# Kernel optimization log

Hardware: AMD Instinct MI355X
Metric: run time of the kernel (lower is better)

## Reference

```python
import jax, jax.numpy as jnp
import numpy as np

SPARSITY = 0.5  # cur_sparsity set during training; 0.0 default would make masking a no-op
WEIGHT_BETA = 1.0
MASK_ALPHA1 = 1.0
MASK_ALPHA2 = 1.0


def binarize(mask_scores, sparsity):
    # SparseBinarizer.forward: prune (set to 0) the `num_prune` smallest scores globally.
    num_prune = int(mask_scores.size * sparsity)  # static: sparsity is a Python float
    flat = mask_scores.reshape(-1)
    prune_idx = jnp.argsort(flat)[:num_prune]
    mask = jnp.ones_like(flat).at[prune_idx].set(0.0)
    return mask.reshape(mask_scores.shape)


def setup_inputs() -> dict:
    key = jax.random.key(0)
    ks = jax.random.split(key, 9)
    out_f, in_f, r = 4096, 4096, 8
    tokens = 8192  # batch 4 * seq 2048
    return {
        "x": jax.random.normal(ks[0], (tokens, in_f), dtype=jnp.float32),
        "weight": jax.random.normal(ks[1], (out_f, in_f), dtype=jnp.float32) * 0.02,
        "bias": jax.random.normal(ks[2], (out_f,), dtype=jnp.float32) * 0.02,
        "weight_U": jax.random.normal(ks[3], (out_f, r), dtype=jnp.float32),
        "weight_V": jnp.zeros((r, in_f), dtype=jnp.float32),
        "mask_scores_A": jax.random.normal(ks[4], (out_f, r), dtype=jnp.float32),
        "mask_scores_B": jnp.zeros((r, in_f), dtype=jnp.float32),
        "mask_scores_R": jnp.zeros((out_f,), dtype=jnp.float32),
        "mask_scores_C": jnp.zeros((in_f,), dtype=jnp.float32),
    }


def reference(x, weight, bias, weight_U, weight_V, mask_scores_A, mask_scores_B,
              mask_scores_R, mask_scores_C):
    # weight = W + beta * U @ V   (low-rank weight reconstruction)
    w = weight + WEIGHT_BETA * (weight_U @ weight_V)
    # mask_scores = |w| + a1 * A @ B + a2 * (R[:,None] + C[None,:])
    mask_scores = (jnp.abs(w)
                   + MASK_ALPHA1 * (mask_scores_A @ mask_scores_B)
                   + MASK_ALPHA2 * (mask_scores_R[:, None] + mask_scores_C[None, :]))
    mask = binarize(mask_scores, SPARSITY)
    masked_weight = mask * w  # [out_f, in_f]
    # nn.Linear: x @ W^T + b
    return x @ masked_weight.T + bias
```

## Files before the change

### kernel.cpp

```cpp
#include <hip/hip_runtime.h>
#include <stdint.h>

#define TOKENS 8192
#define OUT_F  4096
#define IN_F   4096
#define RNK    8
#define KPRUNE 8388608u
#define CAP3   16384u

typedef unsigned short u16;
typedef float  f32x4  __attribute__((ext_vector_type(4)));
typedef short  bf16x8 __attribute__((ext_vector_type(8)));
typedef unsigned short u16x4 __attribute__((ext_vector_type(4)));
typedef unsigned short u16x8 __attribute__((ext_vector_type(8)));

#define XB_OFF    0ull
#define WB_OFF    67108864ull
#define KEYS_OFF  100663296ull
#define CTL_OFF   167772160ull
#define H1_OFF    0
#define H2_OFF    16384
#define SEL_OFF   32768
#define CNT3_OFF  32800
#define LIST3_OFF 32804
#define CTL_ZERO_U32 8201

__device__ __forceinline__ u16 f2bf(float f) {
    uint32_t u = __float_as_uint(f);
    u += 0x7fffu + ((u >> 16) & 1u);
    return (u16)(u >> 16);
}

__device__ __forceinline__ uint32_t fkey(float s) {
    uint32_t u = __float_as_uint(s);
    return (u & 0x80000000u) ? ~u : (u | 0x80000000u);
}

__global__ void convx_kernel(const float* __restrict__ x, u16* __restrict__ xB,
                             uint32_t* __restrict__ ctl)
{
    const int t = threadIdx.x;
    if (blockIdx.x < 34) {
        const int i = blockIdx.x * 256 + t;
        if (i < CTL_ZERO_U32) ctl[i] = 0u;
    }
    const size_t idx = (size_t)blockIdx.x * 256 + t;
    const float4* xv = (const float4*)x;
    float4 a = xv[idx*2];
    float4 b = xv[idx*2 + 1];
    u16x8 o;
    o[0]=f2bf(a.x); o[1]=f2bf(a.y); o[2]=f2bf(a.z); o[3]=f2bf(a.w);
    o[4]=f2bf(b.x); o[5]=f2bf(b.y); o[6]=f2bf(b.z); o[7]=f2bf(b.w);
    *((u16x8*)xB + idx) = o;
}

__global__ void prep_kernel(const float* __restrict__ W, const float* __restrict__ U,
                            const float* __restrict__ V, const float* __restrict__ A,
                            const float* __restrict__ B, const float* __restrict__ R,
                            const float* __restrict__ C, u16* __restrict__ wB,
                            uint32_t* __restrict__ keys, uint32_t* __restrict__ hist1)
{
    __shared__ uint32_t lh[4096];
    const int o0 = blockIdx.x * 2, t = threadIdx.x;
    for (int b = t; b < 4096; b += 256) lh[b] = 0u;
    float uu0[RNK], uu1[RNK], aa0[RNK], aa1[RNK];
#pragma unroll
    for (int r = 0; r < RNK; ++r) {
        uu0[r] = U[o0*RNK + r];       uu1[r] = U[(o0+1)*RNK + r];
        aa0[r] = A[o0*RNK + r];       aa1[r] = A[(o0+1)*RNK + r];
    }
    const float ro0 = R[o0], ro1 = R[o0 + 1];
    __syncthreads();
    for (int j = 0; j < IN_F/1024; ++j) {
        const int i = j*1024 + t*4;
        const float4 cc = *(const float4*)&C[i];
        float4 w0 = *(const float4*)&W[(size_t)o0*IN_F + i];
        float4 w1 = *(const float4*)&W[(size_t)(o0+1)*IN_F + i];
#pragma unroll
        for (int r = 0; r < RNK; ++r) {
            const float4 v4 = *(const float4*)&V[r*IN_F + i];
            const float a0 = uu0[r], a1 = uu1[r];
            w0.x = fmaf(a0, v4.x, w0.x); w0.y = fmaf(a0, v4.y, w0.y);
            w0.z = fmaf(a0, v4.z, w0.z); w0.w = fmaf(a0, v4.w, w0.w);
            w1.x = fmaf(a1, v4.x, w1.x); w1.y = fmaf(a1, v4.y, w1.y);
            w1.z = fmaf(a1, v4.z, w1.z); w1.w = fmaf(a1, v4.w, w1.w);
        }
        float4 s0, s1;
        s0.x = fabsf(w0.x); s0.y = fabsf(w0.y); s0.z = fabsf(w0.z); s0.w = fabsf(w0.w);
        s1.x = fabsf(w1.x); s1.y = fabsf(w1.y); s1.z = fabsf(w1.z); s1.w = fabsf(w1.w);
#pragma unroll
        for (int r = 0; r < RNK; ++r) {
            const float4 b4 = *(const float4*)&B[r*IN_F + i];
            const float a0 = aa0[r], a1 = aa1[r];
            s0.x = fmaf(a0, b4.x, s0.x); s0.y = fmaf(a0, b4.y, s0.y);
            s0.z = fmaf(a0, b4.z, s0.z); s0.w = fmaf(a0, b4.w, s0.w);
            s1.x = fmaf(a1, b4.x, s1.x); s1.y = fmaf(a1, b4.y, s1.y);
            s1.z = fmaf(a1, b4.z, s1.z); s1.w = fmaf(a1, b4.w, s1.w);
        }
        s0.x += ro0 + cc.x; s0.y += ro0 + cc.y; s0.z += ro0 + cc.z; s0.w += ro0 + cc.w;
        s1.x += ro1 + cc.x; s1.y += ro1 + cc.y; s1.z += ro1 + cc.z; s1.w += ro1 + cc.w;
        uint4 k0, k1;
        k0.x = fkey(s0.x); k0.y = fkey(s0.y); k0.z = fkey(s0.z); k0.w = fkey(s0.w);
        k1.x = fkey(s1.x); k1.y = fkey(s1.y); k1.z = fkey(s1.z); k1.w = fkey(s1.w);
        *(uint4*)&keys[(size_t)o0*IN_F + i]     = k0;
        *(uint4*)&keys[(size_t)(o0+1)*IN_F + i] = k1;
        u16x4 b0, b1;
        b0[0]=f2bf(w0.x); b0[1]=f2bf(w0.y); b0[2]=f2bf(w0.z); b0[3]=f2bf(w0.w);
        b1[0]=f2bf(w1.x); b1[1]=f2bf(w1.y); b1[2]=f2bf(w1.z); b1[3]=f2bf(w1.w);
        *(u16x4*)&wB[(size_t)o0*IN_F + i]     = b0;
        *(u16x4*)&wB[(size_t)(o0+1)*IN_F + i] = b1;
        atomicAdd(&lh[k0.x >> 20], 1u); atomicAdd(&lh[k0.y >> 20], 1u);
        atomicAdd(&lh[k0.z >> 20], 1u); atomicAdd(&lh[k0.w >> 20], 1u);
        atomicAdd(&lh[k1.x >> 20], 1u); atomicAdd(&lh[k1.y >> 20], 1u);
        atomicAdd(&lh[k1.z >> 20], 1u); atomicAdd(&lh[k1.w >> 20], 1u);
    }
    __syncthreads();
    for (int b = t; b < 4096; b += 256) { uint32_t c = lh[b]; if (c) atomicAdd(&hist1[b], c); }
}

__global__ void select_kernel(const uint32_t* __restrict__ hist, uint32_t* sel, int mode)
{
    __shared__ uint32_t lh[4096];
    __shared__ uint32_t part[256];
    __shared__ uint32_t sseg[2];
    const int t = threadIdx.x;
    const uint32_t c1v = sel[1];
    const uint32_t k = (mode == 0) ? KPRUNE : (KPRUNE - c1v);
    for (int b = t; b < 4096; b += 256) lh[b] = hist[b];
    __syncthreads();
    uint32_t s = 0;
    for (int j = 0; j < 16; ++j) s += lh[t*16 + j];
    part[t] = s;
    __syncthreads();
    uint32_t pre = 0;
    for (int tt = 0; tt < t; ++tt) pre += part[tt];
    if (pre < k && pre + part[t] >= k) { sseg[0] = (uint32_t)t; sseg[1] = pre; }
    __syncthreads();
    const int seg = (int)sseg[0];
    const uint32_t accb = sseg[1];
    if (t < 16) {
        uint32_t pre2 = 0;
        for (int j = 0; j < t; ++j) pre2 += lh[seg*16 + j];
        const uint32_t c = lh[seg*16 + t];
        const uint32_t below = accb + pre2;
        if (below < k && below + c >= k) {
            const uint32_t bin = (uint32_t)(seg*16 + t);
            if (mode == 0) { sel[0] = bin; sel[1] = below; }
            else           { sel[2] = bin; sel[3] = c1v + below; }
        }
    }
}

__global__ void hist2_kernel(const uint32_t* __restrict__ keys, const uint32_t* __restrict__ sel,
                             uint32_t* __restrict__ hist2)
{
    __shared__ uint32_t lh[4096];
    const int o = blockIdx.x, t = threadIdx.x;
    const uint32_t b1 = sel[0];
    for (int b = t; b < 4096; b += 256) lh[b] = 0u;
    __syncthreads();
    const uint32_t* kp = keys + (size_t)o*IN_F + t*16;
#pragma unroll
    for (int q = 0; q < 4; ++q) {
        uint4 kv = *(const uint4*)(kp + q*4);
        if ((kv.x >> 20) == b1) atomicAdd(&lh[(kv.x >> 8) & 0xFFFu], 1u);
        if ((kv.y >> 20) == b1) atomicAdd(&lh[(kv.y >> 8) & 0xFFFu], 1u);
        if ((kv.z >> 20) == b1) atomicAdd(&lh[(kv.z >> 8) & 0xFFFu], 1u);
        if ((kv.w >> 20) == b1) atomicAdd(&lh[(kv.w >> 8) & 0xFFFu], 1u);
    }
    __syncthreads();
    for (int b = t; b < 4096; b += 256) { uint32_t c = lh[b]; if (c) atomicAdd(&hist2[b], c); }
}

__global__ void apply_kernel(const uint32_t* __restrict__ keys, const uint32_t* __restrict__ sel,
                             u16* __restrict__ wB, uint32_t* __restrict__ cnt3,
                             uint32_t* __restrict__ list3)
{
    const uint32_t pfx = (sel[0] << 12) | sel[2];
    const size_t base = ((size_t)blockIdx.x * 256 + threadIdx.x) * 16;
    uint32_t kv[16];
#pragma unroll
    for (int q = 0; q < 4; ++q) *(uint4*)(kv + q*4) = *(const uint4*)(keys + base + q*4);
    uint4 wraw[2];
    wraw[0] = *(const uint4*)(wB + base);
    wraw[1] = *(const uint4*)(wB + base + 8);
    u16* wv = (u16*)wraw;
#pragma unroll
    for (int e = 0; e < 16; ++e) {
        const uint32_t hi = kv[e] >> 8;
        if (hi < pfx) wv[e] = 0u;
        else if (hi == pfx) {
            uint32_t s = atomicAdd(cnt3, 1u);
            if (s < CAP3) list3[s] = ((uint32_t)(base + e) << 8) | (kv[e] & 0xFFu);
        }
    }
    *(uint4*)(wB + base)     = wraw[0];
    *(uint4*)(wB + base + 8) = wraw[1];
}

__global__ void selfix_kernel(const uint32_t* __restrict__ sel, const uint32_t* __restrict__ cnt3,
                              const uint32_t* __restrict__ list3, u16* __restrict__ wB)
{
    __shared__ uint32_t lst[CAP3];
    __shared__ uint32_t hist[256];
    __shared__ uint32_t sv[2];
    const int t = threadIdx.x;
    uint32_t n = *cnt3; if (n > CAP3) n = CAP3;
    hist[t] = 0u;
    __syncthreads();
    for (uint32_t i = t; i < n; i += 256) {
        const uint32_t e = list3[i];
        lst[i] = e;
        atomicAdd(&hist[e & 0xFFu], 1u);
    }
    __syncthreads();
    const uint32_t k3 = KPRUNE - sel[3];
    uint32_t pre = 0;
    for (int b = 0; b < t; ++b) pre += hist[b];
    if (pre < k3 && pre + hist[t] >= k3) {
        sv[0] = (uint32_t)t;
        sv[1] = k3 - pre;
    }
    __syncthreads();
    const uint32_t b3 = sv[0], p = sv[1];
    for (uint32_t i = t; i < n; i += 256) {
        const uint32_t e = lst[i];
        const uint32_t lo = e & 0xFFu;
        if (lo < b3) { wB[e >> 8] = 0u; continue; }
        if (lo != b3) continue;
        uint32_t rank = 0;
        for (uint32_t j = 0; j < n; ++j) {
            const uint32_t f = lst[j];
            rank += ((f & 0xFFu) == b3 && f < e) ? 1u : 0u;
        }
        if (rank < p) wB[e >> 8] = 0u;
    }
}

#define A0H0   0
#define A0H1_0 16384
#define A0H1_1 32768
#define B0S    49152
#define A1H0   81920
#define A1H1_0 98304
#define A1H1_1 114688
#define B1S    131072

__device__ __forceinline__ void gl_lds16(const char* src, char* dst) {
    __builtin_amdgcn_global_load_lds((const __attribute__((address_space(1))) void*)src,
                                     (__attribute__((address_space(3))) void*)dst, 16, 0, 0);
}

__global__ __launch_bounds__(512, 2) void gemm256_kernel(const u16* __restrict__ xB,
                                                         const u16* __restrict__ wB,
                                                         const float* __restrict__ bias,
                                                         float* __restrict__ out)
{
    __shared__ char ldsc[163840];
    const int t    = threadIdx.x;
    const int lane = t & 63;
    const int wid  = t >> 6;
    const int wm   = wid >> 2;
    const int wn   = wid & 3;
    const int bid  = blockIdx.x;
    const int bn   = bid & 15;
    const int bm   = bid >> 4;

    const int l15 = lane & 15;
    const int kb  = (lane >> 4) << 4;
    const int rowA = 16*wm + l15;
    const int rowB = (wn & 1)*64 + l15;
    const int baseA = rowA*64 + (kb ^ (((rowA >> 1) & 3) << 4));
    const int baseB = rowB*64 + (kb ^ (((rowB >> 1) & 3) << 4));
    const char* aB0 = ldsc + baseA;
    const char* aB1 = ldsc + A1H0 + baseA;
    const char* bB0 = ldsc + B0S + (wn >> 1)*16384 + baseB;
    const char* bB1 = bB0 + (B1S - B0S);

    const int scol = ((t & 3) * 16) ^ (((t >> 3) & 3) << 4);
    const char* pA = (const char*)xB + ((size_t)(bm*256 + (t >> 2))) * (IN_F*2) + scol;
    const char* pB = (const char*)wB + ((size_t)(bn*256 + (t >> 2))) * (IN_F*2) + scol;
    const int tb16 = t * 16;

#define STAGEH(pG, slot, h, tile) do {                                        \
    const char* _s = (pG) + (size_t)(tile)*128 + (size_t)(h)*(128*IN_F*2);    \
    char* _d = ldsc + (slot) + tb16;                                          \
    gl_lds16(_s, _d);                                                         \
    gl_lds16(_s + 64, _d + 8192);                                             \
} while (0)

    f32x4  acc[8][4] = {};
    bf16x8 b[4][2];
    bf16x8 a[2][2];

#define LOADB(bp) do {                                                        \
    _Pragma("unroll") for (int ni = 0; ni < 4; ++ni)                          \
    _Pragma("unroll") for (int kk = 0; kk < 2; ++kk)                          \
        b[ni][kk] = *(const bf16x8*)((bp) + ni*1024 + kk*8192);               \
} while (0)

#define LOADA(ap, slot, q, mo) do {                                           \
    _Pragma("unroll") for (int mm = 0; mm < 2; ++mm)                          \
    _Pragma("unroll") for (int kk = 0; kk < 2; ++kk)                          \
        a[mm][kk] = *(const bf16x8*)((ap) + (slot) +                          \
                      (2*(q)+mm-(mo))*2048 + kk*8192);                        \
} while (0)

#define MFMAQ(q) do {                                                         \
    _Pragma("unroll") for (int mm = 0; mm < 2; ++mm)                          \
    _Pragma("unroll") for (int ni = 0; ni < 4; ++ni)                          \
    _Pragma("unroll") for (int kk = 0; kk < 2; ++kk)                          \
        acc[2*(q)+mm][ni] = __builtin_amdgcn_mfma_f32_16x16x32_bf16(          \
            a[mm][kk], b[ni][kk], acc[2*(q)+mm][ni], 0, 0, 0);                \
} while (0)

#define PH_TAIL(q)                                                            \
    __builtin_amdgcn_s_barrier();                                             \
    asm volatile("s_waitcnt lgkmcnt(0)" ::: "memory");                        \
    __builtin_amdgcn_s_setprio(1);                                            \
    MFMAQ(q);                                                                 \
    __builtin_amdgcn_s_setprio(0);                                            \
    __builtin_amdgcn_s_barrier();

#define STQ(q) do {                                                           \
    _Pragma("unroll") for (int mm = 0; mm < 2; ++mm) {                        \
        const int r0 = orow0 + 32*(2*(q)+mm);                                 \
        _Pragma("unroll") for (int ni = 0; ni < 4; ++ni) {                    \
            f32x4 v = acc[2*(q)+mm][ni];                                      \
            const int col = ocol0 + ni*16;                                    \
            _Pragma("unroll") for (int e = 0; e < 4; ++e)                     \
                out[(size_t)(r0 + e)*OUT_F + col] = v[e] + bv[ni];            \
        }                                                                     \
    }                                                                         \
} while (0)

#define PH_TAIL_ST(q)                                                         \
    __builtin_amdgcn_s_barrier();                                             \
    asm volatile("s_waitcnt lgkmcnt(0)" ::: "memory");                        \
    __builtin_amdgcn_s_setprio(1);                                            \
    MFMAQ(q);                                                                 \
    __builtin_amdgcn_s_setprio(0);                                            \
    STQ(q);                                                                   \
    __builtin_amdgcn_s_barrier();

    STAGEH(pA, A0H1_0, 1, 0);
    STAGEH(pB, B0S,         0, 0);
    STAGEH(pB, B0S + 16384, 1, 0);
    STAGEH(pA, A0H0, 0, 0);
    STAGEH(pA, A1H1_0, 1, 1);
    STAGEH(pB, B1S,         0, 1);
    STAGEH(pB, B1S + 16384, 1, 1);
    STAGEH(pA, A1H0, 0, 1);
    asm volatile("s_waitcnt vmcnt(8)" ::: "memory");
    __builtin_amdgcn_s_barrier();

#pragma unroll 1
    for (int j = 0; j < 31; ++j) {
        const int se = 2*j + 2;
        const int so = 2*j + 3;
        const int pc = j & 1;
        const int a0h1c = pc ? A0H1_1 : A0H1_0;
        const int a0h1n = pc ? A0H1_0 : A0H1_1;
        const int a1h1c = pc ? A1H1_1 : A1H1_0;
        const int a1h1n = pc ? A1H1_0 : A1H1_1;

        LOADB(bB0); LOADA(aB0, A0H0, 0, 0);
        STAGEH(pA, a0h1n, 1, se);
        asm volatile("s_waitcnt lgkmcnt(8)" ::: "memory");
        PH_TAIL(0)
        LOADA(aB0, A0H0, 1, 0);
        STAGEH(pB, B0S, 0, se);
        PH_TAIL(1)
        LOADA(aB0, a0h1c, 2, 4);
        STAGEH(pB, B0S + 16384, 1, se);
        PH_TAIL(2)
        LOADA(aB0, a0h1c, 3, 4);
        STAGEH(pA, A0H0, 0, se);
        asm volatile("s_waitcnt vmcnt(8)" ::: "memory");
        PH_TAIL(3)

        LOADB(bB1); LOADA(aB1, 0, 0, 0);
        STAGEH(pA, a1h1n, 1, so);
        asm volatile("s_waitcnt lgkmcnt(8)" ::: "memory");
        PH_TAIL(0)
        LOADA(aB1, 0, 1, 0);
        STAGEH(pB, B1S, 0, so);
        PH_TAIL(1)
        LOADA(aB1, a1h1c - A1H0, 2, 4);
        STAGEH(pB, B1S + 16384, 1, so);
        PH_TAIL(2)
        LOADA(aB1, a1h1c - A1H0, 3, 4);
        STAGEH(pA, A1H0, 0, so);
        asm volatile("s_waitcnt vmcnt(8)" ::: "memory");
        PH_TAIL(3)
    }

    const int orow0 = bm*256 + 16*wm + ((lane >> 4) << 2);
    const int ocol0 = bn*256 + 64*wn + l15;
    float bv[4];
#pragma unroll
    for (int ni = 0; ni < 4; ++ni) bv[ni] = bias[ocol0 + ni*16];

    LOADB(bB0); LOADA(aB0, A0H0, 0, 0);
    asm volatile("s_waitcnt lgkmcnt(8)" ::: "memory");
    PH_TAIL(0)
    LOADA(aB0, A0H0, 1, 0);
    PH_TAIL(1)
    LOADA(aB0, A0H1_1, 2, 4);
    PH_TAIL(2)
    LOADA(aB0, A0H1_1, 3, 4);
    PH_TAIL(3)

    asm volatile("s_waitcnt vmcnt(0)" ::: "memory");
    __builtin_amdgcn_s_barrier();
    LOADB(bB1); LOADA(aB1, 0, 0, 0);
    asm volatile("s_waitcnt lgkmcnt(8)" ::: "memory");
    PH_TAIL_ST(0)
    LOADA(aB1, 0, 1, 0);
    PH_TAIL_ST(1)
    LOADA(aB1, A1H1_1 - A1H0, 2, 4);
    PH_TAIL_ST(2)
    LOADA(aB1, A1H1_1 - A1H0, 3, 4);
    PH_TAIL_ST(3)

#undef STAGEH
#undef LOADB
#undef LOADA
#undef MFMAQ
#undef PH_TAIL
#undef PH_TAIL_ST
#undef STQ
}

extern "C" void kernel_launch(void* const* d_in, const int* in_sizes, int n_in,
                              void* d_out, int out_size, void* d_ws, size_t ws_size,
                              hipStream_t stream)
{
    const float* x    = (const float*)d_in[0];
    const float* W    = (const float*)d_in[1];
    const float* bias = (const float*)d_in[2];
    const float* U    = (const float*)d_in[3];
    const float* V    = (const float*)d_in[4];
    const float* A    = (const float*)d_in[5];
    const float* B    = (const float*)d_in[6];
    const float* R    = (const float*)d_in[7];
    const float* C    = (const float*)d_in[8];
    float* out = (float*)d_out;

    char* ws = (char*)d_ws;
    u16*      xB    = (u16*)(ws + XB_OFF);
    u16*      wB    = (u16*)(ws + WB_OFF);
    uint32_t* keys  = (uint32_t*)(ws + KEYS_OFF);
    uint32_t* ctl   = (uint32_t*)(ws + CTL_OFF);
    uint32_t* h1    = (uint32_t*)((char*)ctl + H1_OFF);
    uint32_t* h2    = (uint32_t*)((char*)ctl + H2_OFF);
    uint32_t* sel   = (uint32_t*)((char*)ctl + SEL_OFF);
    uint32_t* cnt3  = (uint32_t*)((char*)ctl + CNT3_OFF);
    uint32_t* list3 = (uint32_t*)((char*)ctl + LIST3_OFF);

    convx_kernel<<<TOKENS*IN_F/8/256, 256, 0, stream>>>(x, xB, ctl);
    prep_kernel<<<OUT_F/2, 256, 0, stream>>>(W, U, V, A, B, R, C, wB, keys, h1);
    select_kernel<<<1, 256, 0, stream>>>(h1, sel, 0);
    hist2_kernel<<<OUT_F, 256, 0, stream>>>(keys, sel, h2);
    select_kernel<<<1, 256, 0, stream>>>(h2, sel, 1);
    apply_kernel<<<OUT_F, 256, 0, stream>>>(keys, sel, wB, cnt3, list3);
    selfix_kernel<<<1, 256, 0, stream>>>(sel, cnt3, list3, wB);
    gemm256_kernel<<<(TOKENS/256)*(OUT_F/256), 512, 0, stream>>>(xB, wB, bias, out);
}
```

Measured before the change: 400.4 us.

## Recompute mask scores from inputs instead of storing and rereading key buffer

The 64MB intermediate keys array is removed. Each selection pass (histogram, second histogram, apply) recomputes the low-rank weight and mask scores directly from W, U, V, A, B, R, C. The bf16 weight is now written only once, in the apply pass, which drops the separate write plus read-modify-write of wB. This replaces one 64MB key write and two 64MB key reads with two extra 64MB reads of W and some redundant FMA work.

```diff
diff --git a/kernel.cpp b/kernel.cpp
--- a/kernel.cpp
+++ b/kernel.cpp
@@ -16,8 +16,7 @@
 
 #define XB_OFF    0ull
 #define WB_OFF    67108864ull
-#define KEYS_OFF  100663296ull
-#define CTL_OFF   167772160ull
+#define CTL_OFF   100663296ull
 #define H1_OFF    0
 #define H2_OFF    16384
 #define SEL_OFF   32768
@@ -35,6 +34,56 @@
     uint32_t u = __float_as_uint(s);
     return (u & 0x80000000u) ? ~u : (u | 0x80000000u);
 }
+
+struct S2 { float4 w0, w1; uint4 k0, k1; };
+__device__ __forceinline__ S2 score2(const float* __restrict__ W,
+                                     const float* __restrict__ V,
+                                     const float* __restrict__ B,
+                                     const float* __restrict__ C,
+                                     const float* uu0, const float* uu1,
+                                     const float* aa0, const float* aa1,
+                                     float ro0, float ro1, int o0, int i)
+{
+    const float4 cc = *(const float4*)&C[i];
+    float4 w0 = *(const float4*)&W[(size_t)o0*IN_F + i];
+    float4 w1 = *(const float4*)&W[(size_t)(o0+1)*IN_F + i];
+#pragma unroll
+    for (int r = 0; r < RNK; ++r) {
+        const float4 v4 = *(const float4*)&V[r*IN_F + i];
+        const float a0 = uu0[r], a1 = uu1[r];
+        w0.x = fmaf(a0, v4.x, w0.x); w0.y = fmaf(a0, v4.y, w0.y);
+        w0.z = fmaf(a0, v4.z, w0.z); w0.w = fmaf(a0, v4.w, w0.w);
+        w1.x = fmaf(a1, v4.x, w1.x); w1.y = fmaf(a1, v4.y, w1.y);
+        w1.z = fmaf(a1, v4.z, w1.z); w1.w = fmaf(a1, v4.w, w1.w);
+    }
+    float4 s0, s1;
+    s0.x = fabsf(w0.x); s0.y = fabsf(w0.y); s0.z = fabsf(w0.z); s0.w = fabsf(w0.w);
+    s1.x = fabsf(w1.x); s1.y = fabsf(w1.y); s1.z = fabsf(w1.z); s1.w = fabsf(w1.w);
+#pragma unroll
+    for (int r = 0; r < RNK; ++r) {
+        const float4 b4 = *(const float4*)&B[r*IN_F + i];
+        const float a0 = aa0[r], a1 = aa1[r];
+        s0.x = fmaf(a0, b4.x, s0.x); s0.y = fmaf(a0, b4.y, s0.y);
+        s0.z = fmaf(a0, b4.z, s0.z); s0.w = fmaf(a0, b4.w, s0.w);
+        s1.x = fmaf(a1, b4.x, s1.x); s1.y = fmaf(a1, b4.y, s1.y);
+        s1.z = fmaf(a1, b4.z, s1.z); s1.w = fmaf(a1, b4.w, s1.w);
+    }
+    s0.x += ro0 + cc.x; s0.y += ro0 + cc.y; s0.z += ro0 + cc.z; s0.w += ro0 + cc.w;
+    s1.x += ro1 + cc.x; s1.y += ro1 + cc.y; s1.z += ro1 + cc.z; s1.w += ro1 + cc.w;
+    S2 o;
+    o.w0 = w0; o.w1 = w1;
+    o.k0.x = fkey(s0.x); o.k0.y = fkey(s0.y); o.k0.z = fkey(s0.z); o.k0.w = fkey(s0.w);
+    o.k1.x = fkey(s1.x); o.k1.y = fkey(s1.y); o.k1.z = fkey(s1.z); o.k1.w = fkey(s1.w);
+    return o;
+}
+
+#define LOAD_ROWPARAMS                                                        \
+    float uu0[RNK], uu1[RNK], aa0[RNK], aa1[RNK];                             \
+    _Pragma("unroll") for (int r = 0; r < RNK; ++r) {                         \
+        uu0[r] = U[o0*RNK + r];   uu1[r] = U[(o0+1)*RNK + r];                 \
+        aa0[r] = A[o0*RNK + r];   aa1[r] = A[(o0+1)*RNK + r];                 \
+    }                                                                         \
+    const float ro0 = R[o0], ro1 = R[o0 + 1];
 
 __global__ void convx_kernel(const float* __restrict__ x, u16* __restrict__ xB,
                              uint32_t* __restrict__ ctl)
@@ -57,62 +106,20 @@
 __global__ void prep_kernel(const float* __restrict__ W, const float* __restrict__ U,
                             const float* __restrict__ V, const float* __restrict__ A,
                             const float* __restrict__ B, const float* __restrict__ R,
-                            const float* __restrict__ C, u16* __restrict__ wB,
-                            uint32_t* __restrict__ keys, uint32_t* __restrict__ hist1)
+                            const float* __restrict__ C, uint32_t* __restrict__ hist1)
 {
     __shared__ uint32_t lh[4096];
     const int o0 = blockIdx.x * 2, t = threadIdx.x;
     for (int b = t; b < 4096; b += 256) lh[b] = 0u;
-    float uu0[RNK], uu1[RNK], aa0[RNK], aa1[RNK];
-#pragma unroll
-    for (int r = 0; r < RNK; ++r) {
-        uu0[r] = U[o0*RNK + r];       uu1[r] = U[(o0+1)*RNK + r];
-        aa0[r] = A[o0*RNK + r];       aa1[r] = A[(o0+1)*RNK + r];
-    }
-    const float ro0 = R[o0], ro1 = R[o0 + 1];
+    LOAD_ROWPARAMS
     __syncthreads();
     for (int j = 0; j < IN_F/1024; ++j) {
         const int i = j*1024 + t*4;
-        const float4 cc = *(const float4*)&C[i];
-        float4 w0 = *(const float4*)&W[(size_t)o0*IN_F + i];
-        float4 w1 = *(const float4*)&W[(size_t)(o0+1)*IN_F + i];
-#pragma unroll
-        for (int r = 0; r < RNK; ++r) {
-            const float4 v4 = *(const float4*)&V[r*IN_F + i];
-            const float a0 = uu0[r], a1 = uu1[r];
-            w0.x = fmaf(a0, v4.x, w0.x); w0.y = fmaf(a0, v4.y, w0.y);
-            w0.z = fmaf(a0, v4.z, w0.z); w0.w = fmaf(a0, v4.w, w0.w);
-            w1.x = fmaf(a1, v4.x, w1.x); w1.y = fmaf(a1, v4.y, w1.y);
-            w1.z = fmaf(a1, v4.z, w1.z); w1.w = fmaf(a1, v4.w, w1.w);
-        }
-        float4 s0, s1;
-        s0.x = fabsf(w0.x); s0.y = fabsf(w0.y); s0.z = fabsf(w0.z); s0.w = fabsf(w0.w);
-        s1.x = fabsf(w1.x); s1.y = fabsf(w1.y); s1.z = fabsf(w1.z); s1.w = fabsf(w1.w);
-#pragma unroll
-        for (int r = 0; r < RNK; ++r) {
-            const float4 b4 = *(const float4*)&B[r*IN_F + i];
-            const float a0 = aa0[r], a1 = aa1[r];
-            s0.x = fmaf(a0, b4.x, s0.x); s0.y = fmaf(a0, b4.y, s0.y);
-            s0.z = fmaf(a0, b4.z, s0.z); s0.w = fmaf(a0, b4.w, s0.w);
-            s1.x = fmaf(a1, b4.x, s1.x); s1.y = fmaf(a1, b4.y, s1.y);
-            s1.z = fmaf(a1, b4.z, s1.z); s1.w = fmaf(a1, b4.w, s1.w);
-        }
-        s0.x += ro0 + cc.x; s0.y += ro0 + cc.y; s0.z += ro0 + cc.z; s0.w += ro0 + cc.w;
-        s1.x += ro1 + cc.x; s1.y += ro1 + cc.y; s1.z += ro1 + cc.z; s1.w += ro1 + cc.w;
-        uint4 k0, k1;
-        k0.x = fkey(s0.x); k0.y = fkey(s0.y); k0.z = fkey(s0.z); k0.w = fkey(s0.w);
-        k1.x = fkey(s1.x); k1.y = fkey(s1.y); k1.z = fkey(s1.z); k1.w = fkey(s1.w);
-        *(uint4*)&keys[(size_t)o0*IN_F + i]     = k0;
-        *(uint4*)&keys[(size_t)(o0+1)*IN_F + i] = k1;
-        u16x4 b0, b1;
-        b0[0]=f2bf(w0.x); b0[1]=f2bf(w0.y); b0[2]=f2bf(w0.z); b0[3]=f2bf(w0.w);
-        b1[0]=f2bf(w1.x); b1[1]=f2bf(w1.y); b1[2]=f2bf(w1.z); b1[3]=f2bf(w1.w);
-        *(u16x4*)&wB[(size_t)o0*IN_F + i]     = b0;
-        *(u16x4*)&wB[(size_t)(o0+1)*IN_F + i] = b1;
-        atomicAdd(&lh[k0.x >> 20], 1u); atomicAdd(&lh[k0.y >> 20], 1u);
-        atomicAdd(&lh[k0.z >> 20], 1u); atomicAdd(&lh[k0.w >> 20], 1u);
-        atomicAdd(&lh[k1.x >> 20], 1u); atomicAdd(&lh[k1.y >> 20], 1u);
-        atomicAdd(&lh[k1.z >> 20], 1u); atomicAdd(&lh[k1.w >> 20], 1u);
+        S2 s = score2(W, V, B, C, uu0, uu1, aa0, aa1, ro0, ro1, o0, i);
+        atomicAdd(&lh[s.k0.x >> 20], 1u); atomicAdd(&lh[s.k0.y >> 20], 1u);
+        atomicAdd(&lh[s.k0.z >> 20], 1u); atomicAdd(&lh[s.k0.w >> 20], 1u);
+        atomicAdd(&lh[s.k1.x >> 20], 1u); atomicAdd(&lh[s.k1.y >> 20], 1u);
+        atomicAdd(&lh[s.k1.z >> 20], 1u); atomicAdd(&lh[s.k1.w >> 20], 1u);
     }
     __syncthreads();
     for (int b = t; b < 4096; b += 256) { uint32_t c = lh[b]; if (c) atomicAdd(&hist1[b], c); }
@@ -151,51 +158,73 @@
     }
 }
 
-__global__ void hist2_kernel(const uint32_t* __restrict__ keys, const uint32_t* __restrict__ sel,
-                             uint32_t* __restrict__ hist2)
+__global__ void hist2r_kernel(const float* __restrict__ W, const float* __restrict__ U,
+                              const float* __restrict__ V, const float* __restrict__ A,
+                              const float* __restrict__ B, const float* __restrict__ R,
+                              const float* __restrict__ C, const uint32_t* __restrict__ sel,
+                              uint32_t* __restrict__ hist2)
 {
     __shared__ uint32_t lh[4096];
-    const int o = blockIdx.x, t = threadIdx.x;
+    const int o0 = blockIdx.x * 2, t = threadIdx.x;
     const uint32_t b1 = sel[0];
     for (int b = t; b < 4096; b += 256) lh[b] = 0u;
-    __syncthreads();
-    const uint32_t* kp = keys + (size_t)o*IN_F + t*16;
+    LOAD_ROWPARAMS
+    __syncthreads();
+    for (int j = 0; j < IN_F/1024; ++j) {
+        const int i = j*1024 + t*4;
+        S2 s = score2(W, V, B, C, uu0, uu1, aa0, aa1, ro0, ro1, o0, i);
+        if ((s.k0.x >> 20) == b1) atomicAdd(&lh[(s.k0.x >> 8) & 0xFFFu], 1u);
+        if ((s.k0.y >> 20) == b1) atomicAdd(&lh[(s.k0.y >> 8) & 0xFFFu], 1u);
+        if ((s.k0.z >> 20) == b1) atomicAdd(&lh[(s.k0.z >> 8) & 0xFFFu], 1u);
+        if ((s.k0.w >> 20) == b1) atomicAdd(&lh[(s.k0.w >> 8) & 0xFFFu], 1u);
+        if ((s.k1.x >> 20) == b1) atomicAdd(&lh[(s.k1.x >> 8) & 0xFFFu], 1u);
+        if ((s.k1.y >> 20) == b1) atomicAdd(&lh[(s.k1.y >> 8) & 0xFFFu], 1u);
+        if ((s.k1.z >> 20) == b1) atomicAdd(&lh[(s.k1.z >> 8) & 0xFFFu], 1u);
+        if ((s.k1.w >> 20) == b1) atomicAdd(&lh[(s.k1.w >> 8) & 0xFFFu], 1u);
+    }
+    __syncthreads();
+    for (int b = t; b < 4096; b += 256) { uint32_t c = lh[b]; if (c) atomicAdd(&hist2[b], c); }
+}
+
+__global__ void applyr_kernel(const float* __restrict__ W, const float* __restrict__ U,
+                              const float* __restrict__ V, const float* __restrict__ A,
+                              const float* __restrict__ B, const float* __restrict__ R,
+                              const float* __restrict__ C, const uint32_t* __restrict__ sel,
+                              u16* __restrict__ wB, uint32_t* __restrict__ cnt3,
+                              uint32_t* __restrict__ list3)
+{
+    const int o0 = blockIdx.x * 2, t = threadIdx.x;
+    const uint32_t pfx = (sel[0] << 12) | sel[2];
+    LOAD_ROWPARAMS
+    for (int j = 0; j < IN_F/1024; ++j) {
+        const int i = j*1024 + t*4;
+        S2 s = score2(W, V, B, C, uu0, uu1, aa0, aa1, ro0, ro1, o0, i);
+        const float w0a[4] = {s.w0.x, s.w0.y, s.w0.z, s.w0.w};
+        const float w1a[4] = {s.w1.x, s.w1.y, s.w1.z, s.w1.w};
+        const uint32_t k0a[4] = {s.k0.x, s.k0.y, s.k0.z, s.k0.w};
+        const uint32_t k1a[4] = {s.k1.x, s.k1.y, s.k1.z, s.k1.w};
+        u16x4 b0, b1v;
 #pragma unroll
-    for (int q = 0; q < 4; ++q) {
-        uint4 kv = *(const uint4*)(kp + q*4);
-        if ((kv.x >> 20) == b1) atomicAdd(&lh[(kv.x >> 8) & 0xFFFu], 1u);
-        if ((kv.y >> 20) == b1) atomicAdd(&lh[(kv.y >> 8) & 0xFFFu], 1u);
-        if ((kv.z >> 20) == b1) atomicAdd(&lh[(kv.z >> 8) & 0xFFFu], 1u);
-        if ((kv.w >> 20) == b1) atomicAdd(&lh[(kv.w >> 8) & 0xFFFu], 1u);
-    }
-    __syncthreads();
-    for (int b = t; b < 4096; b += 256) { uint32_t c = lh[b]; if (c) atomicAdd(&hist2[b], c); }
-}
-
-__global__ void apply_kernel(const uint32_t* __restrict__ keys, const uint32_t* __restrict__ sel,
-                             u16* __restrict__ wB, uint32_t* __restrict__ cnt3,
-                             uint32_t* __restrict__ list3)
-{
-    const uint32_t pfx = (sel[0] << 12) | sel[2];
-    const size_t base = ((size_t)blockIdx.x * 256 + threadIdx.x) * 16;
-    uint32_t kv[16];
+        for (int e = 0; e < 4; ++e) {
+            const uint32_t hi = k0a[e] >> 8;
+            b0[e] = (hi < pfx) ? (u16)0 : f2bf(w0a[e]);
+            if (hi == pfx) {
+                uint32_t sl = atomicAdd(cnt3, 1u);
+                if (sl < CAP3) list3[sl] = ((uint32_t)(o0*IN_F + i + e) << 8) | (k0a[e] & 0xFFu);
+            }
+        }
 #pragma unroll
-    for (int q = 0; q < 4; ++q) *(uint4*)(kv + q*4) = *(const uint4*)(keys + base + q*4);
-    uint4 wraw[2];
-    wraw[0] = *(const uint4*)(wB + base);
-    wraw[1] = *(const uint4*)(wB + base + 8);
-    u16* wv = (u16*)wraw;
-#pragma unroll
-    for (int e = 0; e < 16; ++e) {
-        const uint32_t hi = kv[e] >> 8;
-        if (hi < pfx) wv[e] = 0u;
-        else if (hi == pfx) {
-            uint32_t s = atomicAdd(cnt3, 1u);
-            if (s < CAP3) list3[s] = ((uint32_t)(base + e) << 8) | (kv[e] & 0xFFu);
+        for (int e = 0; e < 4; ++e) {
+            const uint32_t hi = k1a[e] >> 8;
+            b1v[e] = (hi < pfx) ? (u16)0 : f2bf(w1a[e]);
+            if (hi == pfx) {
+                uint32_t sl = atomicAdd(cnt3, 1u);
+                if (sl < CAP3) list3[sl] = ((uint32_t)((o0+1)*IN_F + i + e) << 8) | (k1a[e] & 0xFFu);
+            }
         }
-    }
-    *(uint4*)(wB + base)     = wraw[0];
-    *(uint4*)(wB + base + 8) = wraw[1];
+        *(u16x4*)&wB[(size_t)o0*IN_F + i]     = b0;
+        *(u16x4*)&wB[(size_t)(o0+1)*IN_F + i] = b1v;
+    }
 }
 
 __global__ void selfix_kernel(const uint32_t* __restrict__ sel, const uint32_t* __restrict__ cnt3,
@@ -450,7 +479,6 @@
     char* ws = (char*)d_ws;
     u16*      xB    = (u16*)(ws + XB_OFF);
     u16*      wB    = (u16*)(ws + WB_OFF);
-    uint32_t* keys  = (uint32_t*)(ws + KEYS_OFF);
     uint32_t* ctl   = (uint32_t*)(ws + CTL_OFF);
     uint32_t* h1    = (uint32_t*)((char*)ctl + H1_OFF);
     uint32_t* h2    = (uint32_t*)((char*)ctl + H2_OFF);
@@ -459,11 +487,11 @@
     uint32_t* list3 = (uint32_t*)((char*)ctl + LIST3_OFF);
 
     convx_kernel<<<TOKENS*IN_F/8/256, 256, 0, stream>>>(x, xB, ctl);
-    prep_kernel<<<OUT_F/2, 256, 0, stream>>>(W, U, V, A, B, R, C, wB, keys, h1);
+    prep_kernel<<<OUT_F/2, 256, 0, stream>>>(W, U, V, A, B, R, C, h1);
     select_kernel<<<1, 256, 0, stream>>>(h1, sel, 0);
-    hist2_kernel<<<OUT_F, 256, 0, stream>>>(keys, sel, h2);
+    hist2r_kernel<<<OUT_F/2, 256, 0, stream>>>(W, U, V, A, B, R, C, sel, h2);
     select_kernel<<<1, 256, 0, stream>>>(h2, sel, 1);
-    apply_kernel<<<OUT_F, 256, 0, stream>>>(keys, sel, wB, cnt3, list3);
+    applyr_kernel<<<OUT_F/2, 256, 0, stream>>>(W, U, V, A, B, R, C, sel, wB, cnt3, list3);
     selfix_kernel<<<1, 256, 0, stream>>>(sel, cnt3, list3, wB);
     gemm256_kernel<<<(TOKENS/256)*(OUT_F/256), 512, 0, stream>>>(xB, wB, bias, out);
 }
```

Result: faster. 383.7 us (-4.2%).
